# Kernel tuning notes

Hardware: AMD Instinct MI355X
Metric: run time of the kernel (lower is better)

Reference implementation:

```python
import jax, jax.numpy as jnp
import numpy as np

B, S, HID = 2, 2048, 3072
NH, NKV, HD = 24, 8, 128  # num_heads, kv heads, head_dim
G = NH // NKV             # GQA group size = 3
SCALING = HD ** -0.5
LAYER_SCALING = 1.0       # sqrt(layer_number=1)


def setup_inputs() -> dict:
    key = jax.random.key(0)
    ks = jax.random.split(key, 10)
    std = 0.02
    inp = {
        "hidden_states": jax.random.normal(ks[0], (B, S, HID), jnp.float32),
        # additive causal mask: 0 on/below diag, -1e9 above
        "attention_mask": jnp.where(
            jnp.tril(jnp.ones((S, S), bool)), 0.0, -1e9
        ).astype(jnp.float32)[None, None],
        # torch nn.Linear layout: W is [out, in]
        "Wq": jax.random.normal(ks[1], (HID, HID), jnp.float32) * std,
        "bq": jnp.zeros((HID,), jnp.float32),
        "Wk": jax.random.normal(ks[2], (NKV * HD, HID), jnp.float32) * std,
        "bk": jnp.zeros((NKV * HD,), jnp.float32),
        "Wv": jax.random.normal(ks[3], (NKV * HD, HID), jnp.float32) * std,
        "bv": jnp.zeros((NKV * HD,), jnp.float32),
        "Wd": jax.random.normal(ks[4], (HID, HID), jnp.float32) * std,
        "bd": jnp.zeros((HID,), jnp.float32),
    }
    return inp


def reference(hidden_states, attention_mask, Wq, bq, Wk, bk, Wv, bv, Wd, bd):
    b, s, _ = hidden_states.shape
    q = hidden_states @ Wq.T + bq                     # [B,S,HID]
    k = hidden_states @ Wk.T + bk                     # [B,S,NKV*HD]
    v = hidden_states @ Wv.T + bv
    # grouped layout: q [B,NKV,G,S,D]; repeat_interleave(dim=1) == grouped kv head
    q = q.reshape(b, s, NKV, G, HD).transpose(0, 2, 3, 1, 4)
    k = k.reshape(b, s, NKV, HD).transpose(0, 2, 1, 3)  # [B,NKV,S,D]
    v = v.reshape(b, s, NKV, HD).transpose(0, 2, 1, 3)
    scores = jnp.einsum("bhgqd,bhkd->bhgqk", q, k)
    scores = scores * (SCALING / LAYER_SCALING)
    scores = scores + attention_mask[:, :, None]       # broadcast over kv-head/group
    probs = jax.nn.softmax(scores.astype(jnp.float32), axis=-1).astype(scores.dtype)
    ctx = jnp.einsum("bhgqk,bhkd->bhgqd", probs, v)    # [B,NKV,G,S,D]
    # (kv_head, group) flattened == repeat_interleave head ordering
    ctx = ctx.transpose(0, 3, 1, 2, 4).reshape(b, s, HID)
    return ctx @ Wd.T + bd
```

## Files before the change

### kernel.cpp

```cpp
#include <hip/hip_runtime.h>

typedef unsigned short ushort_t;
typedef unsigned int uint32;
typedef __bf16 bf16x8 __attribute__((ext_vector_type(8)));
typedef float f32x4 __attribute__((ext_vector_type(4)));
typedef float f32x16 __attribute__((ext_vector_type(16)));

#define MFMA16(a, b, c) __builtin_amdgcn_mfma_f32_16x16x32_bf16((a), (b), (c), 0, 0, 0)
#define MFMA32(a, b, c) __builtin_amdgcn_mfma_f32_32x32x16_bf16((a), (b), (c), 0, 0, 0)

__device__ __forceinline__ ushort_t f2bf(float f) {
  union { float f; uint32 u; } c; c.f = f;
  uint32 u = c.u;
  u += 0x7fffu + ((u >> 16) & 1u);
  return (ushort_t)(u >> 16);
}

__device__ __forceinline__ void gload_lds16(const void* g, void* l) {
  __builtin_amdgcn_global_load_lds(
      (const __attribute__((address_space(1))) void*)g,
      (__attribute__((address_space(3))) void*)l, 16, 0, 0);
}

__global__ __launch_bounds__(256)
void cvt5_kernel(const float* __restrict__ p0, const float* __restrict__ p1,
                 const float* __restrict__ p2, const float* __restrict__ p3,
                 const float* __restrict__ p4, ushort_t* __restrict__ out) {
  const size_t B0 = 12582912;
  const size_t B1 = B0 + 9437184;
  const size_t B2 = B1 + 3145728;
  const size_t B3 = B2 + 3145728;
  const size_t B4 = B3 + 9437184;
  const size_t step = (size_t)gridDim.x * 256 * 4;
  for (size_t g = ((size_t)blockIdx.x * 256 + threadIdx.x) * 4; g < B4; g += step) {
    const float* src; size_t off;
    if (g < B0)      { src = p0; off = 0;  }
    else if (g < B1) { src = p1; off = B0; }
    else if (g < B2) { src = p2; off = B1; }
    else if (g < B3) { src = p3; off = B2; }
    else             { src = p4; off = B3; }
    float4 v = *(const float4*)(src + (g - off));
    union { uint2 u; ushort_t s[4]; } p;
    p.s[0] = f2bf(v.x); p.s[1] = f2bf(v.y);
    p.s[2] = f2bf(v.z); p.s[3] = f2bf(v.w);
    *(uint2*)(out + g) = p.u;
  }
}

#define GEMM_BODY32(ABASE, WROWBASE, KD)                                        \
  f32x16 acc[2][2] = {};                                                        \
  const int l31 = lane & 31;                                                    \
  const int khb = (lane >> 5) << 4;            \
  const int nk = (KD) >> 6;                                                     \
  for (int kt = 0; kt < nk; ++kt) {                                             \
    _Pragma("unroll")                                                           \
    for (int i = 0; i < 4; ++i) {                                               \
      int o = (i * 256 + tid) * 16;                                             \
      int row = o >> 7;                                                         \
      int src = (o & 127) ^ ((row & 7) << 4);                                   \
      gload_lds16(ABASE + (rowA0 + row) * (KD) + kt * 64 + (src >> 1),          \
                  (char*)As + o);                                               \
      gload_lds16(WROWBASE + (size_t)row * (KD) + kt * 64 + (src >> 1),         \
                  (char*)Bs + o);                                               \
    }                                                                           \
    __syncthreads();                                                            \
    _Pragma("unroll")                                                           \
    for (int ks = 0; ks < 4; ++ks) {                                            \
      bf16x8 af[2], bfr[2];                                                     \
      _Pragma("unroll")                                                         \
      for (int mi = 0; mi < 2; ++mi) {                                          \
        int ar = wr * 64 + mi * 32 + l31;                                       \
        int off = ar * 128 + ((ks * 32 + khb) ^ ((ar & 7) << 4));               \
        af[mi] = *(const bf16x8*)((const char*)As + off);                       \
      }                                                                         \
      _Pragma("unroll")                                                         \
      for (int nj = 0; nj < 2; ++nj) {                                          \
        int br = wc * 64 + nj * 32 + l31;                                       \
        int off = br * 128 + ((ks * 32 + khb) ^ ((br & 7) << 4));               \
        bfr[nj] = *(const bf16x8*)((const char*)Bs + off);                      \
      }                                                                         \
      _Pragma("unroll")                                                         \
      for (int mi = 0; mi < 2; ++mi)                                            \
        _Pragma("unroll")                                                       \
        for (int nj = 0; nj < 2; ++nj)                                          \
          acc[mi][nj] = MFMA32(af[mi], bfr[nj], acc[mi][nj]);                   \
    }                                                                           \
    __syncthreads();                                                            \
  }

__global__ __launch_bounds__(256)
void qkv_gemm_kernel(const ushort_t* __restrict__ A,
                     const ushort_t* __restrict__ Wq, const ushort_t* __restrict__ Wk,
                     const ushort_t* __restrict__ Wv,
                     const float* __restrict__ bq, const float* __restrict__ bk,
                     const float* __restrict__ bv, ushort_t* __restrict__ C)
{
  __shared__ __attribute__((aligned(16))) ushort_t As[128 * 64];
  __shared__ __attribute__((aligned(16))) ushort_t Bs[128 * 64];
  const int tid = threadIdx.x;
  const int lane = tid & 63;
  const int wv_ = tid >> 6;
  const int wr = wv_ >> 1, wc = wv_ & 1;
  const int x = blockIdx.x & 7;
  const int li = blockIdx.x >> 3;
  const int bm = ((x & 1) << 4) | (li & 15);
  const int bn = (x >> 1) * 10 + (li >> 4);

  const ushort_t* Wsrc; const float* bsrc; int nloc;
  if (bn < 24)      { Wsrc = Wq; bsrc = bq; nloc = bn << 7; }
  else if (bn < 32) { Wsrc = Wk; bsrc = bk; nloc = (bn - 24) << 7; }
  else              { Wsrc = Wv; bsrc = bv; nloc = (bn - 32) << 7; }

  const size_t rowA0 = (size_t)bm * 128;
  const ushort_t* Wrow = Wsrc + (size_t)nloc * 3072;

  GEMM_BODY32(A, Wrow, 3072)

  const int rhi = (lane >> 5) << 2;
#pragma unroll
  for (int nj = 0; nj < 2; ++nj) {
    int cl = wc * 64 + nj * 32 + l31;
    float bvl = bsrc[nloc + cl];
    int col = bn * 128 + cl;
#pragma unroll
    for (int mi = 0; mi < 2; ++mi) {
      int row0 = bm * 128 + wr * 64 + mi * 32 + rhi;
#pragma unroll
      for (int r = 0; r < 16; ++r) {
        int rowl = (r & 3) + 8 * (r >> 2);
        C[(size_t)(row0 + rowl) * 5120 + col] = f2bf(acc[mi][nj][r] + bvl);
      }
    }
  }
}

template <bool OUT_F32>
__global__ __launch_bounds__(256)
void gemm_bt_kernel(const ushort_t* __restrict__ A, const ushort_t* __restrict__ W,
                    const float* __restrict__ bias, void* __restrict__ Cv,
                    int N, int Kd, int cbn)
{
  __shared__ __attribute__((aligned(16))) ushort_t As[128 * 64];
  __shared__ __attribute__((aligned(16))) ushort_t Bs[128 * 64];
  const int tid = threadIdx.x;
  const int lane = tid & 63;
  const int wv_ = tid >> 6;
  const int wr = wv_ >> 1, wc = wv_ & 1;
  const int x = blockIdx.x & 7;
  const int li = blockIdx.x >> 3;
  const int bm = ((x & 1) << 4) | (li & 15);
  const int bn = (x >> 1) * cbn + (li >> 4);

  const size_t rowA0 = (size_t)bm * 128;
  const ushort_t* Wrow = W + (size_t)(bn * 128) * Kd;

  GEMM_BODY32(A, Wrow, Kd)

  const int rhi = (lane >> 5) << 2;
#pragma unroll
  for (int nj = 0; nj < 2; ++nj) {
    int col = bn * 128 + wc * 64 + nj * 32 + l31;
    float bvl = bias[col];
#pragma unroll
    for (int mi = 0; mi < 2; ++mi) {
      int row0 = bm * 128 + wr * 64 + mi * 32 + rhi;
#pragma unroll
      for (int r = 0; r < 16; ++r) {
        int rowl = (r & 3) + 8 * (r >> 2);
        float v = acc[mi][nj][r] + bvl;
        if (OUT_F32) ((float*)Cv)[(size_t)(row0 + rowl) * N + col] = v;
        else         ((ushort_t*)Cv)[(size_t)(row0 + rowl) * N + col] = f2bf(v);
      }
    }
  }
}

#define NHEADS 24
#define GRP 3
#define SEQ 2048
#define QSCL 0.12751745f
#define DTHR 8.0f

__device__ __forceinline__ int kperm(int u) {
  return 8 * ((u >> 2) & 3) + 4 * ((u >> 4) & 1) + (u & 3) + 32 * (u >> 5);
}

__global__ __launch_bounds__(256)
void attn_kernel(const ushort_t* __restrict__ QKV, ushort_t* __restrict__ O)
{
  __shared__ __attribute__((aligned(16))) ushort_t Kl[2][64 * 128];
  __shared__ __attribute__((aligned(16))) ushort_t Vt[128 * 64];

  const int tid = threadIdx.x;
  const int lane = tid & 63;
  const int wv = tid >> 6;
  const int l15 = lane & 15, lg = lane >> 4;
  const int bh = blockIdx.x;
  const int qb = 31 - blockIdx.y;
  const int b = bh / NHEADS, h = bh % NHEADS;
  const int kvh = h / GRP;
  const size_t kbase = (size_t)b * SEQ * 5120 + 3072 + (size_t)kvh * 128;
  const size_t vbase = kbase + 1024;
  const int q0 = qb * 64;

  const int kv4 = (tid & 15) * 4;
  const int d8 = (tid >> 4) * 8;

#pragma unroll
  for (int i = 0; i < 4; ++i) {
    int o = (i * 256 + tid) * 16;
    int row = o >> 8;
    int src = (o & 255) ^ ((row & 7) << 4);
    gload_lds16(QKV + kbase + (size_t)kperm(row) * 5120 + (src >> 1),
                (char*)&Kl[0][0] + o);
  }
  uint4 vr0, vr1, vr2, vr3;
  {
    const ushort_t* vg = QKV + vbase + (size_t)kv4 * 5120 + d8;
    vr0 = *(const uint4*)(vg);
    vr1 = *(const uint4*)(vg + 5120);
    vr2 = *(const uint4*)(vg + 10240);
    vr3 = *(const uint4*)(vg + 15360);
  }

  bf16x8 qf[4];
  {
    const ushort_t* qg = QKV + (size_t)(b * SEQ + q0 + wv * 16 + l15) * 5120 + h * 128 + lg * 8;
#pragma unroll
    for (int c = 0; c < 4; ++c) {
      bf16x8 q = *(const bf16x8*)(qg + c * 32);
#pragma unroll
      for (int e = 0; e < 8; ++e) q[e] = (__bf16)((float)q[e] * QSCL);
      qf[c] = q;
    }
  }

  float m_st = -1e30f, l_st = 0.f;
  f32x4 accO[8] = {};

  for (int t = 0; t <= qb; ++t) {
    const int cur = t & 1;
    {
      union { uint4 u; ushort_t s[8]; } L0, L1, L2, L3;
      L0.u = vr0; L1.u = vr1; L2.u = vr2; L3.u = vr3;
#pragma unroll
      for (int dd = 0; dd < 8; ++dd) {
        int d = d8 + dd;
        uint2 w;
        w.x = (uint32)L0.s[dd] | ((uint32)L1.s[dd] << 16);
        w.y = (uint32)L2.s[dd] | ((uint32)L3.s[dd] << 16);
        int swz = ((d & 7) ^ ((d >> 3) & 3)) << 4;
        int off = (d * 128 + kv4 * 2) ^ swz;
        *(uint2*)((char*)Vt + off) = w;
      }
    }
    asm volatile("s_waitcnt lgkmcnt(0)" ::: "memory");
    __builtin_amdgcn_s_barrier();

    if (t < qb) {
      const int kvn = (t + 1) * 64;
#pragma unroll
      for (int i = 0; i < 4; ++i) {
        int o = (i * 256 + tid) * 16;
        int row = o >> 8;
        int src = (o & 255) ^ ((row & 7) << 4);
        gload_lds16(QKV + kbase + (size_t)(kvn + kperm(row)) * 5120 + (src >> 1),
                    (char*)&Kl[cur ^ 1][0] + o);
      }
      const ushort_t* vg = QKV + vbase + (size_t)(kvn + kv4) * 5120 + d8;
      vr0 = *(const uint4*)(vg);
      vr1 = *(const uint4*)(vg + 5120);
      vr2 = *(const uint4*)(vg + 10240);
      vr3 = *(const uint4*)(vg + 15360);
    }

    f32x4 s[4];
    __builtin_amdgcn_s_setprio(1);
#pragma unroll
    for (int n = 0; n < 4; ++n) {
      f32x4 z = {0.f, 0.f, 0.f, 0.f};
      s[n] = z;
#pragma unroll
      for (int c = 0; c < 4; ++c) {
        int row = n * 16 + l15;
        int boff = (row * 256 + c * 64 + lg * 16) ^ ((row & 7) << 4);
        bf16x8 kf = *(const bf16x8*)((const char*)Kl[cur] + boff);
        s[n] = MFMA16(kf, qf[c], s[n]);
      }
    }
    __builtin_amdgcn_s_setprio(0);

    if (t == qb) {
      const int qg_ = wv * 16 + l15;
      const int blg = 8 * lg;
#pragma unroll
      for (int n = 0; n < 4; ++n)
#pragma unroll
        for (int r = 0; r < 4; ++r) {
          int kvr = blg + ((n & 1) << 2) + r + ((n >> 1) << 5);
          if (kvr > qg_) s[n][r] = -1e9f;
        }
    }

    float mx = fmaxf(fmaxf(fmaxf(s[0][0], s[0][1]), fmaxf(s[0][2], s[0][3])),
                     fmaxf(fmaxf(s[1][0], s[1][1]), fmaxf(s[1][2], s[1][3])));
    mx = fmaxf(mx, fmaxf(fmaxf(fmaxf(s[2][0], s[2][1]), fmaxf(s[2][2], s[2][3])),
                         fmaxf(fmaxf(s[3][0], s[3][1]), fmaxf(s[3][2], s[3][3]))));
    mx = fmaxf(mx, __shfl_xor(mx, 16, 64));
    mx = fmaxf(mx, __shfl_xor(mx, 32, 64));

    if (!__all(mx <= m_st + DTHR)) {
      const float mnew = fmaxf(m_st, mx);
      const float alpha = __builtin_amdgcn_exp2f(m_st - mnew);
      m_st = mnew;
      l_st *= alpha;
#pragma unroll
      for (int j = 0; j < 8; ++j)
#pragma unroll
        for (int r = 0; r < 4; ++r) accO[j][r] *= alpha;
    }

    float rsum = 0.f;
#pragma unroll
    for (int n = 0; n < 4; ++n) {
      s[n][0] = __builtin_amdgcn_exp2f(s[n][0] - m_st);
      s[n][1] = __builtin_amdgcn_exp2f(s[n][1] - m_st);
      s[n][2] = __builtin_amdgcn_exp2f(s[n][2] - m_st);
      s[n][3] = __builtin_amdgcn_exp2f(s[n][3] - m_st);
      rsum += (s[n][0] + s[n][1]) + (s[n][2] + s[n][3]);
    }
    rsum += __shfl_xor(rsum, 16, 64);
    rsum += __shfl_xor(rsum, 32, 64);
    l_st += rsum;

#pragma unroll
    for (int c = 0; c < 2; ++c) {
      bf16x8 pb;
#pragma unroll
      for (int j = 0; j < 8; ++j)
        pb[j] = (__bf16)s[(c << 1) | (j >> 2)][j & 3];
      __builtin_amdgcn_s_setprio(1);
#pragma unroll
      for (int j = 0; j < 8; ++j) {
        int d = j * 16 + l15;
        int swz = ((d & 7) ^ ((d >> 3) & 3)) << 4;
        int off = (d * 128 + c * 64 + lg * 16) ^ swz;
        bf16x8 vf = *(const bf16x8*)((const char*)Vt + off);
        accO[j] = MFMA16(vf, pb, accO[j]);
      }
      __builtin_amdgcn_s_setprio(0);
    }
    __builtin_amdgcn_s_barrier();
  }

  const float inv = 1.0f / l_st;
  ushort_t* og = O + (size_t)(b * SEQ + q0 + wv * 16 + l15) * 3072 + h * 128 + lg * 4;
#pragma unroll
  for (int j = 0; j < 8; ++j) {
    union { __bf16 h[4]; uint2 u; } w;
    w.h[0] = (__bf16)(accO[j][0] * inv);
    w.h[1] = (__bf16)(accO[j][1] * inv);
    w.h[2] = (__bf16)(accO[j][2] * inv);
    w.h[3] = (__bf16)(accO[j][3] * inv);
    *(uint2*)(og + j * 16) = w.u;
  }
}

extern "C" void kernel_launch(void* const* d_in, const int* in_sizes, int n_in,
                              void* d_out, int out_size, void* d_ws, size_t ws_size,
                              hipStream_t stream) {
  const float* hs = (const float*)d_in[0];
  const float* Wq = (const float*)d_in[2];
  const float* bq = (const float*)d_in[3];
  const float* Wk = (const float*)d_in[4];
  const float* bk = (const float*)d_in[5];
  const float* Wv = (const float*)d_in[6];
  const float* bv = (const float*)d_in[7];
  const float* Wd = (const float*)d_in[8];
  const float* bd = (const float*)d_in[9];
  float* out = (float*)d_out;

  const size_t N_HS = (size_t)4096 * 3072;
  const size_t N_WQ = (size_t)3072 * 3072;
  const size_t N_WK = (size_t)1024 * 3072;

  ushort_t* hs_bf = (ushort_t*)d_ws;
  ushort_t* Wq_bf = hs_bf + N_HS;
  ushort_t* Wk_bf = Wq_bf + N_WQ;
  ushort_t* Wv_bf = Wk_bf + N_WK;
  ushort_t* Wd_bf = Wv_bf + N_WK;
  ushort_t* QKVw  = Wd_bf + N_WQ;
  ushort_t* Cw    = hs_bf;

  cvt5_kernel<<<dim3(2048), dim3(256), 0, stream>>>(hs, Wq, Wk, Wv, Wd, hs_bf);
  qkv_gemm_kernel<<<dim3(1280), dim3(256), 0, stream>>>(hs_bf, Wq_bf, Wk_bf, Wv_bf,
                                                        bq, bk, bv, QKVw);
  attn_kernel<<<dim3(48, 32), dim3(256), 0, stream>>>(QKVw, Cw);
  gemm_bt_kernel<true><<<dim3(24 * 32), dim3(256), 0, stream>>>(Cw, Wd_bf, bd, out,
                                                                3072, 3072, 6);
}
```

Before: 379.3 us.

## Double attention query tile to 128 rows with 512-thread blocks sharing K/V loads

The attention kernel now processes 128 query rows per block with 8 waves instead of 64 rows with 4 waves, so each K/V tile staged in LDS is reused by twice as many query rows. Global loads and the V transpose are split across 512 threads. Waves whose rows lie entirely before a KV tile skip its compute, and causal masking is applied per wave. The trade-offs are fewer blocks, more load imbalance along the causal diagonal (some waves idle at the barrier during the last tiles), and tighter register budgets under the 512-thread launch bound.

```diff
diff --git a/kernel.cpp b/kernel.cpp
--- a/kernel.cpp
+++ b/kernel.cpp
@@ -185,7 +185,7 @@
   return 8 * ((u >> 2) & 3) + 4 * ((u >> 4) & 1) + (u & 3) + 32 * (u >> 5);
 }
 
-__global__ __launch_bounds__(256)
+__global__ __launch_bounds__(512)
 void attn_kernel(const ushort_t* __restrict__ QKV, ushort_t* __restrict__ O)
 {
   __shared__ __attribute__((aligned(16))) ushort_t Kl[2][64 * 128];
@@ -196,36 +196,36 @@
   const int wv = tid >> 6;
   const int l15 = lane & 15, lg = lane >> 4;
   const int bh = blockIdx.x;
-  const int qb = 31 - blockIdx.y;
+  const int qc = 15 - blockIdx.y;
   const int b = bh / NHEADS, h = bh % NHEADS;
   const int kvh = h / GRP;
   const size_t kbase = (size_t)b * SEQ * 5120 + 3072 + (size_t)kvh * 128;
   const size_t vbase = kbase + 1024;
-  const int q0 = qb * 64;
-
-  const int kv4 = (tid & 15) * 4;
-  const int d8 = (tid >> 4) * 8;
-
-#pragma unroll
-  for (int i = 0; i < 4; ++i) {
-    int o = (i * 256 + tid) * 16;
+  const int q0 = qc * 128;
+  const int nt = 2 * qc + 2;
+  const int qwbase = q0 + wv * 16;
+
+  const int kv2 = (tid & 31) * 2;
+  const int d8 = (tid >> 5) * 8;
+
+#pragma unroll
+  for (int i = 0; i < 2; ++i) {
+    int o = (i * 512 + tid) * 16;
     int row = o >> 8;
     int src = (o & 255) ^ ((row & 7) << 4);
     gload_lds16(QKV + kbase + (size_t)kperm(row) * 5120 + (src >> 1),
                 (char*)&Kl[0][0] + o);
   }
-  uint4 vr0, vr1, vr2, vr3;
+  uint4 vr0, vr1;
   {
-    const ushort_t* vg = QKV + vbase + (size_t)kv4 * 5120 + d8;
+    const ushort_t* vg = QKV + vbase + (size_t)kv2 * 5120 + d8;
     vr0 = *(const uint4*)(vg);
     vr1 = *(const uint4*)(vg + 5120);
-    vr2 = *(const uint4*)(vg + 10240);
-    vr3 = *(const uint4*)(vg + 15360);
   }
 
   bf16x8 qf[4];
   {
-    const ushort_t* qg = QKV + (size_t)(b * SEQ + q0 + wv * 16 + l15) * 5120 + h * 128 + lg * 8;
+    const ushort_t* qg = QKV + (size_t)(b * SEQ + qwbase + l15) * 5120 + h * 128 + lg * 8;
 #pragma unroll
     for (int c = 0; c < 4; ++c) {
       bf16x8 q = *(const bf16x8*)(qg + c * 32);
@@ -238,123 +238,121 @@
   float m_st = -1e30f, l_st = 0.f;
   f32x4 accO[8] = {};
 
-  for (int t = 0; t <= qb; ++t) {
+  for (int t = 0; t < nt; ++t) {
     const int cur = t & 1;
     {
-      union { uint4 u; ushort_t s[8]; } L0, L1, L2, L3;
-      L0.u = vr0; L1.u = vr1; L2.u = vr2; L3.u = vr3;
+      union { uint4 u; ushort_t s[8]; } L0, L1;
+      L0.u = vr0; L1.u = vr1;
 #pragma unroll
       for (int dd = 0; dd < 8; ++dd) {
         int d = d8 + dd;
-        uint2 w;
-        w.x = (uint32)L0.s[dd] | ((uint32)L1.s[dd] << 16);
-        w.y = (uint32)L2.s[dd] | ((uint32)L3.s[dd] << 16);
+        uint32 w = (uint32)L0.s[dd] | ((uint32)L1.s[dd] << 16);
         int swz = ((d & 7) ^ ((d >> 3) & 3)) << 4;
-        int off = (d * 128 + kv4 * 2) ^ swz;
-        *(uint2*)((char*)Vt + off) = w;
+        int off = (d * 128 + kv2 * 2) ^ swz;
+        *(uint32*)((char*)Vt + off) = w;
       }
     }
     asm volatile("s_waitcnt lgkmcnt(0)" ::: "memory");
     __builtin_amdgcn_s_barrier();
 
-    if (t < qb) {
+    if (t < nt - 1) {
       const int kvn = (t + 1) * 64;
 #pragma unroll
-      for (int i = 0; i < 4; ++i) {
-        int o = (i * 256 + tid) * 16;
+      for (int i = 0; i < 2; ++i) {
+        int o = (i * 512 + tid) * 16;
         int row = o >> 8;
         int src = (o & 255) ^ ((row & 7) << 4);
         gload_lds16(QKV + kbase + (size_t)(kvn + kperm(row)) * 5120 + (src >> 1),
                     (char*)&Kl[cur ^ 1][0] + o);
       }
-      const ushort_t* vg = QKV + vbase + (size_t)(kvn + kv4) * 5120 + d8;
+      const ushort_t* vg = QKV + vbase + (size_t)((t + 1) * 64 + kv2) * 5120 + d8;
       vr0 = *(const uint4*)(vg);
       vr1 = *(const uint4*)(vg + 5120);
-      vr2 = *(const uint4*)(vg + 10240);
-      vr3 = *(const uint4*)(vg + 15360);
-    }
-
-    f32x4 s[4];
-    __builtin_amdgcn_s_setprio(1);
-#pragma unroll
-    for (int n = 0; n < 4; ++n) {
-      f32x4 z = {0.f, 0.f, 0.f, 0.f};
-      s[n] = z;
-#pragma unroll
-      for (int c = 0; c < 4; ++c) {
-        int row = n * 16 + l15;
-        int boff = (row * 256 + c * 64 + lg * 16) ^ ((row & 7) << 4);
-        bf16x8 kf = *(const bf16x8*)((const char*)Kl[cur] + boff);
-        s[n] = MFMA16(kf, qf[c], s[n]);
-      }
-    }
-    __builtin_amdgcn_s_setprio(0);
-
-    if (t == qb) {
-      const int qg_ = wv * 16 + l15;
-      const int blg = 8 * lg;
-#pragma unroll
-      for (int n = 0; n < 4; ++n)
-#pragma unroll
-        for (int r = 0; r < 4; ++r) {
-          int kvr = blg + ((n & 1) << 2) + r + ((n >> 1) << 5);
-          if (kvr > qg_) s[n][r] = -1e9f;
+    }
+
+    if (t * 64 <= qwbase + 15) {
+      f32x4 s[4];
+      __builtin_amdgcn_s_setprio(1);
+#pragma unroll
+      for (int n = 0; n < 4; ++n) {
+        f32x4 z = {0.f, 0.f, 0.f, 0.f};
+        s[n] = z;
+#pragma unroll
+        for (int c = 0; c < 4; ++c) {
+          int row = n * 16 + l15;
+          int boff = (row * 256 + c * 64 + lg * 16) ^ ((row & 7) << 4);
+          bf16x8 kf = *(const bf16x8*)((const char*)Kl[cur] + boff);
+          s[n] = MFMA16(kf, qf[c], s[n]);
         }
-    }
-
-    float mx = fmaxf(fmaxf(fmaxf(s[0][0], s[0][1]), fmaxf(s[0][2], s[0][3])),
-                     fmaxf(fmaxf(s[1][0], s[1][1]), fmaxf(s[1][2], s[1][3])));
-    mx = fmaxf(mx, fmaxf(fmaxf(fmaxf(s[2][0], s[2][1]), fmaxf(s[2][2], s[2][3])),
-                         fmaxf(fmaxf(s[3][0], s[3][1]), fmaxf(s[3][2], s[3][3]))));
-    mx = fmaxf(mx, __shfl_xor(mx, 16, 64));
-    mx = fmaxf(mx, __shfl_xor(mx, 32, 64));
-
-    if (!__all(mx <= m_st + DTHR)) {
-      const float mnew = fmaxf(m_st, mx);
-      const float alpha = __builtin_amdgcn_exp2f(m_st - mnew);
-      m_st = mnew;
-      l_st *= alpha;
-#pragma unroll
-      for (int j = 0; j < 8; ++j)
-#pragma unroll
-        for (int r = 0; r < 4; ++r) accO[j][r] *= alpha;
-    }
-
-    float rsum = 0.f;
-#pragma unroll
-    for (int n = 0; n < 4; ++n) {
-      s[n][0] = __builtin_amdgcn_exp2f(s[n][0] - m_st);
-      s[n][1] = __builtin_amdgcn_exp2f(s[n][1] - m_st);
-      s[n][2] = __builtin_amdgcn_exp2f(s[n][2] - m_st);
-      s[n][3] = __builtin_amdgcn_exp2f(s[n][3] - m_st);
-      rsum += (s[n][0] + s[n][1]) + (s[n][2] + s[n][3]);
-    }
-    rsum += __shfl_xor(rsum, 16, 64);
-    rsum += __shfl_xor(rsum, 32, 64);
-    l_st += rsum;
-
-#pragma unroll
-    for (int c = 0; c < 2; ++c) {
-      bf16x8 pb;
-#pragma unroll
-      for (int j = 0; j < 8; ++j)
-        pb[j] = (__bf16)s[(c << 1) | (j >> 2)][j & 3];
-      __builtin_amdgcn_s_setprio(1);
-#pragma unroll
-      for (int j = 0; j < 8; ++j) {
-        int d = j * 16 + l15;
-        int swz = ((d & 7) ^ ((d >> 3) & 3)) << 4;
-        int off = (d * 128 + c * 64 + lg * 16) ^ swz;
-        bf16x8 vf = *(const bf16x8*)((const char*)Vt + off);
-        accO[j] = MFMA16(vf, pb, accO[j]);
       }
       __builtin_amdgcn_s_setprio(0);
+
+      if (t * 64 + 63 > qwbase) {
+        const int qrel = qwbase + l15 - t * 64;
+        const int blg = 8 * lg;
+#pragma unroll
+        for (int n = 0; n < 4; ++n)
+#pragma unroll
+          for (int r = 0; r < 4; ++r) {
+            int kvr = blg + ((n & 1) << 2) + r + ((n >> 1) << 5);
+            if (kvr > qrel) s[n][r] = -1e9f;
+          }
+      }
+
+      float mx = fmaxf(fmaxf(fmaxf(s[0][0], s[0][1]), fmaxf(s[0][2], s[0][3])),
+                       fmaxf(fmaxf(s[1][0], s[1][1]), fmaxf(s[1][2], s[1][3])));
+      mx = fmaxf(mx, fmaxf(fmaxf(fmaxf(s[2][0], s[2][1]), fmaxf(s[2][2], s[2][3])),
+                           fmaxf(fmaxf(s[3][0], s[3][1]), fmaxf(s[3][2], s[3][3]))));
+      mx = fmaxf(mx, __shfl_xor(mx, 16, 64));
+      mx = fmaxf(mx, __shfl_xor(mx, 32, 64));
+
+      if (!__all(mx <= m_st + DTHR)) {
+        const float mnew = fmaxf(m_st, mx);
+        const float alpha = __builtin_amdgcn_exp2f(m_st - mnew);
+        m_st = mnew;
+        l_st *= alpha;
+#pragma unroll
+        for (int j = 0; j < 8; ++j)
+#pragma unroll
+          for (int r = 0; r < 4; ++r) accO[j][r] *= alpha;
+      }
+
+      float rsum = 0.f;
+#pragma unroll
+      for (int n = 0; n < 4; ++n) {
+        s[n][0] = __builtin_amdgcn_exp2f(s[n][0] - m_st);
+        s[n][1] = __builtin_amdgcn_exp2f(s[n][1] - m_st);
+        s[n][2] = __builtin_amdgcn_exp2f(s[n][2] - m_st);
+        s[n][3] = __builtin_amdgcn_exp2f(s[n][3] - m_st);
+        rsum += (s[n][0] + s[n][1]) + (s[n][2] + s[n][3]);
+      }
+      rsum += __shfl_xor(rsum, 16, 64);
+      rsum += __shfl_xor(rsum, 32, 64);
+      l_st += rsum;
+
+#pragma unroll
+      for (int c = 0; c < 2; ++c) {
+        bf16x8 pb;
+#pragma unroll
+        for (int j = 0; j < 8; ++j)
+          pb[j] = (__bf16)s[(c << 1) | (j >> 2)][j & 3];
+        __builtin_amdgcn_s_setprio(1);
+#pragma unroll
+        for (int j = 0; j < 8; ++j) {
+          int d = j * 16 + l15;
+          int swz = ((d & 7) ^ ((d >> 3) & 3)) << 4;
+          int off = (d * 128 + c * 64 + lg * 16) ^ swz;
+          bf16x8 vf = *(const bf16x8*)((const char*)Vt + off);
+          accO[j] = MFMA16(vf, pb, accO[j]);
+        }
+        __builtin_amdgcn_s_setprio(0);
+      }
     }
     __builtin_amdgcn_s_barrier();
   }
 
   const float inv = 1.0f / l_st;
-  ushort_t* og = O + (size_t)(b * SEQ + q0 + wv * 16 + l15) * 3072 + h * 128 + lg * 4;
+  ushort_t* og = O + (size_t)(b * SEQ + qwbase + l15) * 3072 + h * 128 + lg * 4;
 #pragma unroll
   for (int j = 0; j < 8; ++j) {
     union { __bf16 h[4]; uint2 u; } w;
@@ -395,7 +393,7 @@
   cvt5_kernel<<<dim3(2048), dim3(256), 0, stream>>>(hs, Wq, Wk, Wv, Wd, hs_bf);
   qkv_gemm_kernel<<<dim3(1280), dim3(256), 0, stream>>>(hs_bf, Wq_bf, Wk_bf, Wv_bf,
                                                         bq, bk, bv, QKVw);
-  attn_kernel<<<dim3(48, 32), dim3(256), 0, stream>>>(QKVw, Cw);
+  attn_kernel<<<dim3(48, 16), dim3(512), 0, stream>>>(QKVw, Cw);
   gemm_bt_kernel<true><<<dim3(24 * 32), dim3(256), 0, stream>>>(Cw, Wd_bf, bd, out,
                                                                 3072, 3072, 6);
 }
```

Result: no change. 384.8 us (+1.5%).
